# Kernel tuning notes

Hardware: AMD Instinct MI355X
Metric: run time of the kernel (lower is better)

Reference implementation:

```python
import jax, jax.numpy as jnp
import numpy as np

EPS = 1e-7
ALPHA, GAMMA = 1.0, 2.0
W_CLASS, W_BBOX, W_GIOU, W_CUT = 1.0, 5.0, 2.0, 3.0
FN_PENALTY = 10.0
N = 4194304


def setup_inputs() -> dict:
    key = jax.random.key(0)
    k = jax.random.split(key, 6)
    return {
        "pred_logits": jax.random.normal(k[0], (N, 4), dtype=jnp.float32),
        "target_labels": jax.random.randint(k[1], (N,), 0, 4, dtype=jnp.int64),
        "pred_boxes": jax.random.uniform(k[2], (N, 4), dtype=jnp.float32),
        "target_boxes": jax.random.uniform(k[3], (N, 4), dtype=jnp.float32),
        "cutting_logits": jax.random.normal(k[4], (N,), dtype=jnp.float32),
        "cutting_targets": (jax.random.uniform(k[5], (N,)) < 0.3).astype(jnp.float32),
    }


def _focal_loss(logits, labels):
    # F.cross_entropy per-sample, then focal reweighting
    logp = jax.nn.log_softmax(logits, axis=-1)
    ce = -jnp.take_along_axis(logp, labels[:, None], axis=-1)[:, 0]
    pt = jnp.exp(-ce)
    return jnp.mean(ALPHA * (1.0 - pt) ** GAMMA * ce)


def _validate_and_fix(boxes):
    # _validate_and_fix_boxes: clamp(min=0) for rows with x1>x2 or y1>y2
    invalid = (boxes[:, 0] > boxes[:, 2]) | (boxes[:, 1] > boxes[:, 3])
    boxes = jnp.where(invalid[:, None], jnp.maximum(boxes, 0.0), boxes)
    # _fix_invalid_boxes inside generalized_box_iou: x2>=x1+1e-6, y2>=y1+1e-6
    x1, y1, x2, y2 = boxes[:, 0], boxes[:, 1], boxes[:, 2], boxes[:, 3]
    x2 = jnp.maximum(x2, x1 + 1e-6)
    y2 = jnp.maximum(y2, y1 + 1e-6)
    return jnp.stack([x1, y1, x2, y2], axis=1)


def _giou_loss(pred_boxes, target_boxes):
    # Matched-pair GIoU: same math as diag(generalized_box_iou(p, t)),
    # computed elementwise instead of materializing the [N,N] matrix.
    b1 = _validate_and_fix(pred_boxes)
    b2 = _validate_and_fix(target_boxes)
    area1 = (b1[:, 2] - b1[:, 0]) * (b1[:, 3] - b1[:, 1])
    area2 = (b2[:, 2] - b2[:, 0]) * (b2[:, 3] - b2[:, 1])
    lt = jnp.maximum(b1[:, :2], b2[:, :2])
    rb = jnp.minimum(b1[:, 2:], b2[:, 2:])
    wh = jnp.maximum(rb - lt, 0.0)
    inter = wh[:, 0] * wh[:, 1]
    union = area1 + area2 - inter
    iou = inter / (union + EPS)
    lt_e = jnp.minimum(b1[:, :2], b2[:, :2])
    rb_e = jnp.maximum(b1[:, 2:], b2[:, 2:])
    wh_e = jnp.maximum(rb_e - lt_e, 0.0)
    enclosing = wh_e[:, 0] * wh_e[:, 1]
    giou = iou - (enclosing - union) / (enclosing + EPS)
    return jnp.mean(jnp.maximum(1.0 - giou, 0.0))


def _weighted_bce(logits, targets):
    # BCEWithLogits, stable form
    bce = jnp.maximum(logits, 0.0) - logits * targets + jnp.log1p(jnp.exp(-jnp.abs(logits)))
    probs = jax.nn.sigmoid(logits)
    fn_mask = (targets == 1.0) & (probs < 0.5)
    weights = jnp.where(fn_mask, FN_PENALTY, 1.0)
    return jnp.mean(bce * weights)


def reference(pred_logits, target_labels, pred_boxes, target_boxes, cutting_logits, cutting_targets):
    loss_class = jnp.maximum(_focal_loss(pred_logits, target_labels), 0.0)
    loss_bbox = jnp.maximum(jnp.mean(jnp.abs(pred_boxes - target_boxes)), 0.0)
    loss_giou = jnp.maximum(_giou_loss(pred_boxes, target_boxes), 0.0)
    loss_cutting = jnp.maximum(_weighted_bce(cutting_logits, cutting_targets), 0.0)
    total = (W_CLASS * loss_class + W_BBOX * loss_bbox
             + W_GIOU * loss_giou + W_CUT * loss_cutting)
    return total, loss_class, loss_bbox, loss_giou, loss_cutting
```

## Files before the change

kernel.cpp:

```cpp
#include <hip/hip_runtime.h>
#include <math.h>

#define EPS 1e-7f
#define FN_PENALTY 10.0f
#define BLOCK 256
#define ROWS_PER_THREAD 8

__device__ __forceinline__ float waveReduceSum(float v) {
    #pragma unroll
    for (int off = 32; off > 0; off >>= 1)
        v += __shfl_down(v, off, 64);
    return v;
}

__device__ __forceinline__ float4 validate_fix(float4 b) {
    bool invalid = (b.x > b.z) || (b.y > b.w);
    if (invalid) {
        b.x = fmaxf(b.x, 0.0f);
        b.y = fmaxf(b.y, 0.0f);
        b.z = fmaxf(b.z, 0.0f);
        b.w = fmaxf(b.w, 0.0f);
    }
    b.z = fmaxf(b.z, b.x + 1e-6f);
    b.w = fmaxf(b.w, b.y + 1e-6f);
    return b;
}

__device__ __forceinline__ void accum_row(
    float4 lg, int lbl, float4 pb, float4 tb, float cl, float ct,
    float& s_class, float& s_bbox, float& s_giou, float& s_cut)
{
    float l0 = lg.x, l1 = lg.y, l2 = lg.z, l3 = lg.w;
    float m = fmaxf(fmaxf(l0, l1), fmaxf(l2, l3));
    float se = __expf(l0 - m) + __expf(l1 - m) + __expf(l2 - m) + __expf(l3 - m);
    float lse = m + __logf(se);
    lbl &= 3;
    float lsel = (lbl == 0) ? l0 : (lbl == 1) ? l1 : (lbl == 2) ? l2 : l3;
    float ce = lse - lsel;
    float pt = __expf(-ce);
    float om = 1.0f - pt;
    s_class += om * om * ce;

    s_bbox += fabsf(pb.x - tb.x) + fabsf(pb.y - tb.y)
            + fabsf(pb.z - tb.z) + fabsf(pb.w - tb.w);

    float4 b1 = validate_fix(pb);
    float4 b2 = validate_fix(tb);
    float area1 = (b1.z - b1.x) * (b1.w - b1.y);
    float area2 = (b2.z - b2.x) * (b2.w - b2.y);
    float ltx = fmaxf(b1.x, b2.x), lty = fmaxf(b1.y, b2.y);
    float rbx = fminf(b1.z, b2.z), rby = fminf(b1.w, b2.w);
    float iw = fmaxf(rbx - ltx, 0.0f), ih = fmaxf(rby - lty, 0.0f);
    float inter = iw * ih;
    float uni = area1 + area2 - inter;
    float iou = inter / (uni + EPS);
    float ex1 = fminf(b1.x, b2.x), ey1 = fminf(b1.y, b2.y);
    float ex2 = fmaxf(b1.z, b2.z), ey2 = fmaxf(b1.w, b2.w);
    float ew = fmaxf(ex2 - ex1, 0.0f), eh = fmaxf(ey2 - ey1, 0.0f);
    float enc = ew * eh;
    float giou = iou - (enc - uni) / (enc + EPS);
    s_giou += fmaxf(1.0f - giou, 0.0f);

    float bce = fmaxf(cl, 0.0f) - cl * ct + log1pf(__expf(-fabsf(cl)));
    float prob = 1.0f / (1.0f + __expf(-cl));
    float w = ((ct == 1.0f) && (prob < 0.5f)) ? FN_PENALTY : 1.0f;
    s_cut += bce * w;
}

__global__ __launch_bounds__(BLOCK) void loss_reduce(
    const float4* __restrict__ pred_logits,
    const int*    __restrict__ labels,
    const float4* __restrict__ pred_boxes,
    const float4* __restrict__ target_boxes,
    const float*  __restrict__ cut_logits,
    const float*  __restrict__ cut_targets,
    float4* __restrict__ block_out, int n)
{
    float s_class = 0.0f, s_bbox = 0.0f, s_giou = 0.0f, s_cut = 0.0f;
    const int tid    = blockIdx.x * BLOCK + threadIdx.x;
    const int stride = gridDim.x * BLOCK;

    if (tid + (ROWS_PER_THREAD - 1) * stride < n && (long)stride * ROWS_PER_THREAD >= n) {
        float4 lg[ROWS_PER_THREAD], pb[ROWS_PER_THREAD], tb[ROWS_PER_THREAD];
        int   lb[ROWS_PER_THREAD];
        float cl[ROWS_PER_THREAD], ct[ROWS_PER_THREAD];
        #pragma unroll
        for (int j = 0; j < ROWS_PER_THREAD; ++j) {
            int i = tid + j * stride;
            lg[j] = pred_logits[i];
            lb[j] = labels[i];
            pb[j] = pred_boxes[i];
            tb[j] = target_boxes[i];
            cl[j] = cut_logits[i];
            ct[j] = cut_targets[i];
        }
        #pragma unroll
        for (int j = 0; j < ROWS_PER_THREAD; ++j)
            accum_row(lg[j], lb[j], pb[j], tb[j], cl[j], ct[j],
                      s_class, s_bbox, s_giou, s_cut);
    } else {
        for (int i = tid; i < n; i += stride)
            accum_row(pred_logits[i], labels[i], pred_boxes[i], target_boxes[i],
                      cut_logits[i], cut_targets[i],
                      s_class, s_bbox, s_giou, s_cut);
    }

    s_class = waveReduceSum(s_class);
    s_bbox  = waveReduceSum(s_bbox);
    s_giou  = waveReduceSum(s_giou);
    s_cut   = waveReduceSum(s_cut);

    __shared__ float red[4][4];
    const int lane = threadIdx.x & 63;
    const int wave = threadIdx.x >> 6;
    if (lane == 0) {
        red[wave][0] = s_class;
        red[wave][1] = s_bbox;
        red[wave][2] = s_giou;
        red[wave][3] = s_cut;
    }
    __syncthreads();
    if (threadIdx.x == 0) {
        float4 r;
        r.x = red[0][0] + red[1][0] + red[2][0] + red[3][0];
        r.y = red[0][1] + red[1][1] + red[2][1] + red[3][1];
        r.z = red[0][2] + red[1][2] + red[2][2] + red[3][2];
        r.w = red[0][3] + red[1][3] + red[2][3] + red[3][3];
        block_out[blockIdx.x] = r;
    }
}

__global__ __launch_bounds__(BLOCK) void finalize_kernel(
    const float4* __restrict__ block_out, int nblocks,
    float* __restrict__ out, float inv_n)
{
    float c = 0.0f, b = 0.0f, g = 0.0f, u = 0.0f;
    for (int i = threadIdx.x; i < nblocks; i += BLOCK) {
        float4 r = block_out[i];
        c += r.x; b += r.y; g += r.z; u += r.w;
    }
    c = waveReduceSum(c);
    b = waveReduceSum(b);
    g = waveReduceSum(g);
    u = waveReduceSum(u);

    __shared__ float red[4][4];
    const int lane = threadIdx.x & 63;
    const int wave = threadIdx.x >> 6;
    if (lane == 0) {
        red[wave][0] = c; red[wave][1] = b; red[wave][2] = g; red[wave][3] = u;
    }
    __syncthreads();
    if (threadIdx.x == 0) {
        float sc = red[0][0] + red[1][0] + red[2][0] + red[3][0];
        float sb = red[0][1] + red[1][1] + red[2][1] + red[3][1];
        float sg = red[0][2] + red[1][2] + red[2][2] + red[3][2];
        float su = red[0][3] + red[1][3] + red[2][3] + red[3][3];
        float lc   = fmaxf(sc * inv_n, 0.0f);
        float lb   = fmaxf(sb * inv_n * 0.25f, 0.0f);
        float lg   = fmaxf(sg * inv_n, 0.0f);
        float lcut = fmaxf(su * inv_n, 0.0f);
        float total = 1.0f * lc + 5.0f * lb + 2.0f * lg + 3.0f * lcut;
        out[0] = total;
        out[1] = lc;
        out[2] = lb;
        out[3] = lg;
        out[4] = lcut;
    }
}

extern "C" void kernel_launch(void* const* d_in, const int* in_sizes, int n_in,
                              void* d_out, int out_size, void* d_ws, size_t ws_size,
                              hipStream_t stream) {
    const float4* pred_logits  = (const float4*)d_in[0];
    const int*    labels       = (const int*)d_in[1];
    const float4* pred_boxes   = (const float4*)d_in[2];
    const float4* target_boxes = (const float4*)d_in[3];
    const float*  cut_logits   = (const float*)d_in[4];
    const float*  cut_targets  = (const float*)d_in[5];
    float4* ws  = (float4*)d_ws;
    float*  out = (float*)d_out;
    const int n = in_sizes[1];

    int grid = (n + BLOCK * ROWS_PER_THREAD - 1) / (BLOCK * ROWS_PER_THREAD);
    if (grid < 1) grid = 1;

    loss_reduce<<<grid, BLOCK, 0, stream>>>(pred_logits, labels, pred_boxes,
                                            target_boxes, cut_logits, cut_targets,
                                            ws, n);
    finalize_kernel<<<1, BLOCK, 0, stream>>>(ws, grid, out, 1.0f / (float)n);
}
```

Before: 245.0 us.

## Use one row per thread with a three-stage partial-sum reduction

The main kernel now processes a single row per thread, launching N/256 blocks instead of batching eight rows per thread. To absorb the much larger count of partials, a 64-block intermediate reduce kernel is added, and the final kernel shrinks to a single wave. The BCE term uses __logf(1+x) instead of log1pf, and the sigmoid is replaced by a sign test on the logit. This trades per-thread memory-level parallelism for more blocks, adds an extra launch and more partial-sum traffic, and slightly lowers log accuracy for small arguments.

```diff
diff --git a/kernel.cpp b/kernel.cpp
--- a/kernel.cpp
+++ b/kernel.cpp
@@ -4,7 +4,6 @@
 #define EPS 1e-7f
 #define FN_PENALTY 10.0f
 #define BLOCK 256
-#define ROWS_PER_THREAD 8
 
 __device__ __forceinline__ float waveReduceSum(float v) {
     #pragma unroll
@@ -61,50 +60,15 @@
     float giou = iou - (enc - uni) / (enc + EPS);
     s_giou += fmaxf(1.0f - giou, 0.0f);
 
-    float bce = fmaxf(cl, 0.0f) - cl * ct + log1pf(__expf(-fabsf(cl)));
-    float prob = 1.0f / (1.0f + __expf(-cl));
-    float w = ((ct == 1.0f) && (prob < 0.5f)) ? FN_PENALTY : 1.0f;
+    float bce = fmaxf(cl, 0.0f) - cl * ct + __logf(1.0f + __expf(-fabsf(cl)));
+    float w = ((ct == 1.0f) && (cl < 0.0f)) ? FN_PENALTY : 1.0f;
     s_cut += bce * w;
 }
 
-__global__ __launch_bounds__(BLOCK) void loss_reduce(
-    const float4* __restrict__ pred_logits,
-    const int*    __restrict__ labels,
-    const float4* __restrict__ pred_boxes,
-    const float4* __restrict__ target_boxes,
-    const float*  __restrict__ cut_logits,
-    const float*  __restrict__ cut_targets,
-    float4* __restrict__ block_out, int n)
+__device__ __forceinline__ void block_reduce_store(
+    float s_class, float s_bbox, float s_giou, float s_cut,
+    float4* __restrict__ out_slot)
 {
-    float s_class = 0.0f, s_bbox = 0.0f, s_giou = 0.0f, s_cut = 0.0f;
-    const int tid    = blockIdx.x * BLOCK + threadIdx.x;
-    const int stride = gridDim.x * BLOCK;
-
-    if (tid + (ROWS_PER_THREAD - 1) * stride < n && (long)stride * ROWS_PER_THREAD >= n) {
-        float4 lg[ROWS_PER_THREAD], pb[ROWS_PER_THREAD], tb[ROWS_PER_THREAD];
-        int   lb[ROWS_PER_THREAD];
-        float cl[ROWS_PER_THREAD], ct[ROWS_PER_THREAD];
-        #pragma unroll
-        for (int j = 0; j < ROWS_PER_THREAD; ++j) {
-            int i = tid + j * stride;
-            lg[j] = pred_logits[i];
-            lb[j] = labels[i];
-            pb[j] = pred_boxes[i];
-            tb[j] = target_boxes[i];
-            cl[j] = cut_logits[i];
-            ct[j] = cut_targets[i];
-        }
-        #pragma unroll
-        for (int j = 0; j < ROWS_PER_THREAD; ++j)
-            accum_row(lg[j], lb[j], pb[j], tb[j], cl[j], ct[j],
-                      s_class, s_bbox, s_giou, s_cut);
-    } else {
-        for (int i = tid; i < n; i += stride)
-            accum_row(pred_logits[i], labels[i], pred_boxes[i], target_boxes[i],
-                      cut_logits[i], cut_targets[i],
-                      s_class, s_bbox, s_giou, s_cut);
-    }
-
     s_class = waveReduceSum(s_class);
     s_bbox  = waveReduceSum(s_bbox);
     s_giou  = waveReduceSum(s_giou);
@@ -126,40 +90,58 @@
         r.y = red[0][1] + red[1][1] + red[2][1] + red[3][1];
         r.z = red[0][2] + red[1][2] + red[2][2] + red[3][2];
         r.w = red[0][3] + red[1][3] + red[2][3] + red[3][3];
-        block_out[blockIdx.x] = r;
+        *out_slot = r;
     }
 }
 
-__global__ __launch_bounds__(BLOCK) void finalize_kernel(
-    const float4* __restrict__ block_out, int nblocks,
-    float* __restrict__ out, float inv_n)
+__global__ __launch_bounds__(BLOCK) void loss_reduce(
+    const float4* __restrict__ pred_logits,
+    const int*    __restrict__ labels,
+    const float4* __restrict__ pred_boxes,
+    const float4* __restrict__ target_boxes,
+    const float*  __restrict__ cut_logits,
+    const float*  __restrict__ cut_targets,
+    float4* __restrict__ block_out, int n)
+{
+    const int i = blockIdx.x * BLOCK + threadIdx.x;
+    float s_class = 0.0f, s_bbox = 0.0f, s_giou = 0.0f, s_cut = 0.0f;
+    if (i < n) {
+        accum_row(pred_logits[i], labels[i], pred_boxes[i], target_boxes[i],
+                  cut_logits[i], cut_targets[i],
+                  s_class, s_bbox, s_giou, s_cut);
+    }
+    block_reduce_store(s_class, s_bbox, s_giou, s_cut, &block_out[blockIdx.x]);
+}
+
+__global__ __launch_bounds__(BLOCK) void reduce_partials(
+    const float4* __restrict__ in, int n, float4* __restrict__ out)
 {
     float c = 0.0f, b = 0.0f, g = 0.0f, u = 0.0f;
-    for (int i = threadIdx.x; i < nblocks; i += BLOCK) {
-        float4 r = block_out[i];
+    for (int i = blockIdx.x * BLOCK + threadIdx.x; i < n; i += gridDim.x * BLOCK) {
+        float4 r = in[i];
+        c += r.x; b += r.y; g += r.z; u += r.w;
+    }
+    block_reduce_store(c, b, g, u, &out[blockIdx.x]);
+}
+
+__global__ void finalize_kernel(const float4* __restrict__ in, int n,
+                                float* __restrict__ out, float inv_n)
+{
+    const int lane = threadIdx.x & 63;
+    float c = 0.0f, b = 0.0f, g = 0.0f, u = 0.0f;
+    for (int i = lane; i < n; i += 64) {
+        float4 r = in[i];
         c += r.x; b += r.y; g += r.z; u += r.w;
     }
     c = waveReduceSum(c);
     b = waveReduceSum(b);
     g = waveReduceSum(g);
     u = waveReduceSum(u);
-
-    __shared__ float red[4][4];
-    const int lane = threadIdx.x & 63;
-    const int wave = threadIdx.x >> 6;
     if (lane == 0) {
-        red[wave][0] = c; red[wave][1] = b; red[wave][2] = g; red[wave][3] = u;
-    }
-    __syncthreads();
-    if (threadIdx.x == 0) {
-        float sc = red[0][0] + red[1][0] + red[2][0] + red[3][0];
-        float sb = red[0][1] + red[1][1] + red[2][1] + red[3][1];
-        float sg = red[0][2] + red[1][2] + red[2][2] + red[3][2];
-        float su = red[0][3] + red[1][3] + red[2][3] + red[3][3];
-        float lc   = fmaxf(sc * inv_n, 0.0f);
-        float lb   = fmaxf(sb * inv_n * 0.25f, 0.0f);
-        float lg   = fmaxf(sg * inv_n, 0.0f);
-        float lcut = fmaxf(su * inv_n, 0.0f);
+        float lc   = fmaxf(c * inv_n, 0.0f);
+        float lb   = fmaxf(b * inv_n * 0.25f, 0.0f);
+        float lg   = fmaxf(g * inv_n, 0.0f);
+        float lcut = fmaxf(u * inv_n, 0.0f);
         float total = 1.0f * lc + 5.0f * lb + 2.0f * lg + 3.0f * lcut;
         out[0] = total;
         out[1] = lc;
@@ -178,15 +160,18 @@
     const float4* target_boxes = (const float4*)d_in[3];
     const float*  cut_logits   = (const float*)d_in[4];
     const float*  cut_targets  = (const float*)d_in[5];
-    float4* ws  = (float4*)d_ws;
+    float4* ws4 = (float4*)d_ws;
     float*  out = (float*)d_out;
     const int n = in_sizes[1];
 
-    int grid = (n + BLOCK * ROWS_PER_THREAD - 1) / (BLOCK * ROWS_PER_THREAD);
-    if (grid < 1) grid = 1;
+    const int grid1 = (n + BLOCK - 1) / BLOCK;
+    const int grid2 = 64;
+    float4* part1 = ws4;
+    float4* part2 = ws4 + grid1;
 
-    loss_reduce<<<grid, BLOCK, 0, stream>>>(pred_logits, labels, pred_boxes,
-                                            target_boxes, cut_logits, cut_targets,
-                                            ws, n);
-    finalize_kernel<<<1, BLOCK, 0, stream>>>(ws, grid, out, 1.0f / (float)n);
+    loss_reduce<<<grid1, BLOCK, 0, stream>>>(pred_logits, labels, pred_boxes,
+                                             target_boxes, cut_logits, cut_targets,
+                                             part1, n);
+    reduce_partials<<<grid2, BLOCK, 0, stream>>>(part1, grid1, part2);
+    finalize_kernel<<<1, 64, 0, stream>>>(part2, grid2, out, 1.0f / (float)n);
 }
```

New measurement: 234.0 us. -4.5%, faster.
